# Performance work log

Hardware: AMD Instinct MI355X
Metric: run time of the kernel (lower is better)

Reference implementation:

```python
import jax, jax.numpy as jnp
import numpy as np

N_NODES = 4096
HIDDEN = 64
N_REL = 8
N_LAYERS = 2


def setup_inputs() -> dict:
    key = jax.random.key(0)
    k0, k1, k2, k3, k4 = jax.random.split(key, 5)
    node_embed = jax.random.normal(k0, (N_NODES + 1, HIDDEN), dtype=jnp.float32)
    w_self = jax.random.normal(k1, (N_LAYERS, HIDDEN, HIDDEN), dtype=jnp.float32) * 0.02
    w_rel = jax.random.normal(k2, (N_LAYERS, N_REL, HIDDEN, HIDDEN), dtype=jnp.float32) * 0.02
    # dense per-relation adjacency buffer [R, N, N]
    rel_adj = jax.random.uniform(k3, (N_REL, N_NODES, N_NODES), dtype=jnp.float32)
    keyword_ids = jax.random.randint(k4, (64, 32), 0, N_NODES + 1)  # pad id == N_NODES
    return {"node_embed": node_embed, "w_self": w_self, "w_rel": w_rel,
            "rel_adj": rel_adj, "keyword_ids": keyword_ids}


def reference(node_embed, w_self, w_rel, rel_adj, keyword_ids):
    num_nodes = rel_adj.shape[1]
    h = node_embed[:num_nodes]  # [N, D]
    for l in range(w_self.shape[0]):
        out = h @ w_self[l]                                   # self loop [N, D]
        msg = jnp.einsum('rnm,md->rnd', rel_adj, h)           # per-relation aggregation
        out = out + jnp.einsum('rnd,rde->ne', msg, w_rel[l])  # per-relation projection, summed over r
        h = jax.nn.relu(out)
    pad = jnp.zeros((1, h.shape[1]), dtype=h.dtype)
    full_plus_pad = jnp.concatenate([h, pad], axis=0)  # [N+1, D]
    return full_plus_pad[keyword_ids]                  # [B, K, D]
```

## Files before the change

kernel.cpp:

```cpp
#include <hip/hip_runtime.h>

#define N_NODES 4096
#define HID 64
#define NH (N_NODES * HID)

typedef float f32x4 __attribute__((ext_vector_type(4)));
typedef short s16x4 __attribute__((ext_vector_type(4)));
typedef short s16x8 __attribute__((ext_vector_type(8)));

__device__ __forceinline__ short f2bf(float f) {
    union { float f; unsigned u; } v; v.f = f;
    unsigned r = v.u + 0x7fffu + ((v.u >> 16) & 1u);
    return (short)(r >> 16);
}

__global__ __launch_bounds__(256) void proj_kernel(
    const float* __restrict__ h, const float* __restrict__ w_self_l,
    const float* __restrict__ w_rel_l, float* __restrict__ S,
    short* __restrict__ BT)
{
    __shared__ float hs[64][65];
    __shared__ float wt[64][64];
    const int tid = threadIdx.x;
    const int mb = blockIdx.x;
    const int p = blockIdx.y;
    const float* w = (p < 8) ? (w_rel_l + p * 64 * 64) : w_self_l;

    #pragma unroll
    for (int i = 0; i < 4; ++i) {
        int idx4 = tid + 256 * i;
        int row = idx4 >> 4, c = idx4 & 15;
        float4 v = *((const float4*)(h + (size_t)(mb * 64 + row) * HID) + c);
        hs[row][c * 4 + 0] = v.x; hs[row][c * 4 + 1] = v.y;
        hs[row][c * 4 + 2] = v.z; hs[row][c * 4 + 3] = v.w;
    }
    #pragma unroll
    for (int i = 0; i < 4; ++i) {
        int idx4 = tid + 256 * i;
        ((float4*)wt)[idx4] = ((const float4*)w)[idx4];
    }
    __syncthreads();

    const int m = tid & 63;
    const int eb = (tid >> 6) * 16;
    float acc[16];
    #pragma unroll
    for (int j = 0; j < 16; ++j) acc[j] = 0.f;

    #pragma unroll 4
    for (int d = 0; d < 64; ++d) {
        float hv = hs[m][d];
        const float4* wr = (const float4*)&wt[d][eb];
        float4 w0 = wr[0], w1 = wr[1], w2 = wr[2], w3 = wr[3];
        acc[0]  += hv * w0.x; acc[1]  += hv * w0.y; acc[2]  += hv * w0.z; acc[3]  += hv * w0.w;
        acc[4]  += hv * w1.x; acc[5]  += hv * w1.y; acc[6]  += hv * w1.z; acc[7]  += hv * w1.w;
        acc[8]  += hv * w2.x; acc[9]  += hv * w2.y; acc[10] += hv * w2.z; acc[11] += hv * w2.w;
        acc[12] += hv * w3.x; acc[13] += hv * w3.y; acc[14] += hv * w3.z; acc[15] += hv * w3.w;
    }

    if (p < 8) {
        #pragma unroll
        for (int j = 0; j < 16; ++j)
            BT[(size_t)(p * 64 + eb + j) * N_NODES + mb * 64 + m] = f2bf(acc[j]);
    } else {
        #pragma unroll
        for (int j = 0; j < 16; ++j)
            S[(size_t)(mb * 64 + m) * HID + eb + j] = acc[j];
    }
}

__global__ __launch_bounds__(256, 4) void gemm_kernel(
    const float* __restrict__ A, const short* __restrict__ BT,
    float* __restrict__ msg)
{
    __shared__ __attribute__((aligned(16))) short As[2][64 * 72];
    __shared__ __attribute__((aligned(16))) short Bs[2][64 * 72];

    const int tid = threadIdx.x;
    const int gid = blockIdx.x;
    const int r  = gid & 7;
    const int rb = (gid >> 3) & 63;
    const int ks = gid >> 9;
    const int wave = tid >> 6, lane = tid & 63;
    const int quad = lane >> 4, l16 = lane & 15;

    const int rA = tid >> 4, cA = tid & 15;
    const int rB = tid >> 3, cB = tid & 7;
    const float* Ag = A  + ((size_t)r * N_NODES + rb * 64) * N_NODES + ks * 2048;
    const short* Bg = BT + ((size_t)r * 64) * N_NODES + ks * 2048;

    f32x4 acc[4];
    #pragma unroll
    for (int nb = 0; nb < 4; ++nb) acc[nb] = (f32x4){0.f, 0.f, 0.f, 0.f};

    f32x4 a_nx[4];
    s16x8 b_nx[2];
    auto load_tile = [&](int t) {
        const int k0 = t * 64;
        #pragma unroll
        for (int j = 0; j < 4; ++j)
            a_nx[j] = __builtin_nontemporal_load(
                (const f32x4*)(Ag + (size_t)(rA + 16 * j) * N_NODES + k0 + cA * 4));
        #pragma unroll
        for (int j = 0; j < 2; ++j)
            b_nx[j] = *(const s16x8*)(Bg + (size_t)(rB + 32 * j) * N_NODES + k0 + cB * 8);
    };
    auto write_tile = [&](int b) {
        #pragma unroll
        for (int j = 0; j < 4; ++j) {
            s16x4 av;
            av[0] = f2bf(a_nx[j][0]); av[1] = f2bf(a_nx[j][1]);
            av[2] = f2bf(a_nx[j][2]); av[3] = f2bf(a_nx[j][3]);
            *(s16x4*)&As[b][(rA + 16 * j) * 72 + cA * 4] = av;
        }
        #pragma unroll
        for (int j = 0; j < 2; ++j)
            *(s16x8*)&Bs[b][(rB + 32 * j) * 72 + cB * 8] = b_nx[j];
    };

    load_tile(0);
    write_tile(0);
    load_tile(1);
    asm volatile("s_waitcnt lgkmcnt(0)" ::: "memory");
    __builtin_amdgcn_s_barrier();

    #pragma unroll 2
    for (int t = 0; t < 32; ++t) {
        const int b = t & 1;
        #pragma unroll
        for (int s = 0; s < 2; ++s) {
            s16x8 af = *(const s16x8*)&As[b][(wave * 16 + l16) * 72 + s * 32 + quad * 8];
            #pragma unroll
            for (int nb = 0; nb < 4; ++nb) {
                s16x8 bfr = *(const s16x8*)&Bs[b][(nb * 16 + l16) * 72 + s * 32 + quad * 8];
                acc[nb] = __builtin_amdgcn_mfma_f32_16x16x32_bf16(af, bfr, acc[nb], 0, 0, 0);
            }
        }
        if (t < 31) {
            __builtin_amdgcn_sched_barrier(0);
            write_tile(b ^ 1);
            if (t < 30) load_tile(t + 2);
            asm volatile("s_waitcnt lgkmcnt(0)" ::: "memory");
            __builtin_amdgcn_s_barrier();
        }
    }

    float* mo = msg + ((size_t)(r * 2 + ks)) * NH;
    #pragma unroll
    for (int nb = 0; nb < 4; ++nb) {
        #pragma unroll
        for (int i = 0; i < 4; ++i) {
            int orow = rb * 64 + wave * 16 + quad * 4 + i;
            mo[(size_t)orow * HID + nb * 16 + l16] = acc[nb][i];
        }
    }
}

__global__ __launch_bounds__(256) void relu_kernel(
    const float* __restrict__ S, const float* __restrict__ msg, float* __restrict__ hout)
{
    int i = blockIdx.x * 256 + threadIdx.x;
    float4 s = ((const float4*)S)[i];
    #pragma unroll
    for (int p = 0; p < 16; ++p) {
        float4 m = ((const float4*)(msg + (size_t)p * NH))[i];
        s.x += m.x; s.y += m.y; s.z += m.z; s.w += m.w;
    }
    float4 o;
    o.x = fmaxf(s.x, 0.f); o.y = fmaxf(s.y, 0.f);
    o.z = fmaxf(s.z, 0.f); o.w = fmaxf(s.w, 0.f);
    ((float4*)hout)[i] = o;
}

__global__ __launch_bounds__(256) void gather_kernel(
    const float* __restrict__ h2, const int* __restrict__ kw, float* __restrict__ out)
{
    int e = blockIdx.x * 256 + threadIdx.x;
    int ki = e >> 6, d = e & 63;
    int id = kw[ki];
    out[e] = ((unsigned)id < (unsigned)N_NODES) ? h2[(size_t)id * HID + d] : 0.f;
}

extern "C" void kernel_launch(void* const* d_in, const int* in_sizes, int n_in,
                              void* d_out, int out_size, void* d_ws, size_t ws_size,
                              hipStream_t stream) {
    const float* node_embed = (const float*)d_in[0];
    const float* w_self     = (const float*)d_in[1];
    const float* w_rel      = (const float*)d_in[2];
    const float* rel_adj    = (const float*)d_in[3];
    const int*   kw         = (const int*)d_in[4];
    float* out = (float*)d_out;

    float* msg = (float*)d_ws;
    float* S   = msg + 16 * NH;
    float* h1  = S + NH;
    float* h2  = h1 + NH;
    short* BT  = (short*)(h2 + NH);

    const float* hin = node_embed;
    float* houts[2] = {h1, h2};
    for (int l = 0; l < 2; ++l) {
        proj_kernel<<<dim3(64, 9), 256, 0, stream>>>(
            hin, w_self + (size_t)l * 64 * 64, w_rel + (size_t)l * 8 * 64 * 64, S, BT);
        gemm_kernel<<<1024, 256, 0, stream>>>(rel_adj, BT, msg);
        relu_kernel<<<256, 256, 0, stream>>>(S, msg, houts[l]);
        hin = houts[l];
    }
    gather_kernel<<<512, 256, 0, stream>>>(h2, kw, out);
}
```

Before: 821.0 us.

## Drop split-K in adjacency GEMM, stream 16-row phases through full K

```diff
diff --git a/kernel.cpp b/kernel.cpp
--- a/kernel.cpp
+++ b/kernel.cpp
@@ -3,6 +3,7 @@
 #define N_NODES 4096
 #define HID 64
 #define NH (N_NODES * HID)
+#define NPART 8
 
 typedef float f32x4 __attribute__((ext_vector_type(4)));
 typedef short s16x4 __attribute__((ext_vector_type(4)));
@@ -69,53 +70,51 @@
     }
 }
 
-__global__ __launch_bounds__(256, 4) void gemm_kernel(
+__global__ __launch_bounds__(256, 3) void gemm_kernel(
     const float* __restrict__ A, const short* __restrict__ BT,
     float* __restrict__ msg)
 {
-    __shared__ __attribute__((aligned(16))) short As[2][64 * 72];
-    __shared__ __attribute__((aligned(16))) short Bs[2][64 * 72];
+    __shared__ __attribute__((aligned(16))) short As[2][16 * 136];
+    __shared__ __attribute__((aligned(16))) short Bs[2][64 * 136];
 
     const int tid = threadIdx.x;
     const int gid = blockIdx.x;
     const int r  = gid & 7;
-    const int rb = (gid >> 3) & 63;
-    const int ks = gid >> 9;
+    const int rb = gid >> 3;
     const int wave = tid >> 6, lane = tid & 63;
     const int quad = lane >> 4, l16 = lane & 15;
 
     const int rA = tid >> 4, cA = tid & 15;
-    const int rB = tid >> 3, cB = tid & 7;
-    const float* Ag = A  + ((size_t)r * N_NODES + rb * 64) * N_NODES + ks * 2048;
-    const short* Bg = BT + ((size_t)r * 64) * N_NODES + ks * 2048;
-
-    f32x4 acc[4];
-    #pragma unroll
-    for (int nb = 0; nb < 4; ++nb) acc[nb] = (f32x4){0.f, 0.f, 0.f, 0.f};
-
-    f32x4 a_nx[4];
-    s16x8 b_nx[2];
-    auto load_tile = [&](int t) {
-        const int k0 = t * 64;
-        #pragma unroll
-        for (int j = 0; j < 4; ++j)
-            a_nx[j] = __builtin_nontemporal_load(
-                (const f32x4*)(Ag + (size_t)(rA + 16 * j) * N_NODES + k0 + cA * 4));
-        #pragma unroll
-        for (int j = 0; j < 2; ++j)
-            b_nx[j] = *(const s16x8*)(Bg + (size_t)(rB + 32 * j) * N_NODES + k0 + cB * 8);
+    const int rB = tid >> 2, cB = tid & 3;
+    const float* Ag = A  + ((size_t)r * N_NODES + rb * 64) * N_NODES;
+    const short* Bg = BT + (size_t)r * 64 * N_NODES;
+
+    f32x4 acc = (f32x4){0.f, 0.f, 0.f, 0.f};
+
+    f32x4 a_nx[2];
+    s16x8 b_nx[4];
+    auto load_tile = [&](int u) {
+        const int ph = u >> 5;
+        const int k0 = (u & 31) * 128;
+        #pragma unroll
+        for (int s = 0; s < 2; ++s)
+            a_nx[s] = __builtin_nontemporal_load(
+                (const f32x4*)(Ag + (size_t)(ph * 16 + rA) * N_NODES + k0 + cA * 4 + s * 64));
+        #pragma unroll
+        for (int s = 0; s < 4; ++s)
+            b_nx[s] = *(const s16x8*)(Bg + (size_t)rB * N_NODES + k0 + cB * 8 + s * 32);
     };
     auto write_tile = [&](int b) {
         #pragma unroll
-        for (int j = 0; j < 4; ++j) {
+        for (int s = 0; s < 2; ++s) {
             s16x4 av;
-            av[0] = f2bf(a_nx[j][0]); av[1] = f2bf(a_nx[j][1]);
-            av[2] = f2bf(a_nx[j][2]); av[3] = f2bf(a_nx[j][3]);
-            *(s16x4*)&As[b][(rA + 16 * j) * 72 + cA * 4] = av;
-        }
-        #pragma unroll
-        for (int j = 0; j < 2; ++j)
-            *(s16x8*)&Bs[b][(rB + 32 * j) * 72 + cB * 8] = b_nx[j];
+            av[0] = f2bf(a_nx[s][0]); av[1] = f2bf(a_nx[s][1]);
+            av[2] = f2bf(a_nx[s][2]); av[3] = f2bf(a_nx[s][3]);
+            *(s16x4*)&As[b][rA * 136 + cA * 4 + s * 64] = av;
+        }
+        #pragma unroll
+        for (int s = 0; s < 4; ++s)
+            *(s16x8*)&Bs[b][rB * 136 + cB * 8 + s * 32] = b_nx[s];
     };
 
     load_tile(0);
@@ -124,36 +123,34 @@
     asm volatile("s_waitcnt lgkmcnt(0)" ::: "memory");
     __builtin_amdgcn_s_barrier();
 
+    float* mo = msg + (size_t)r * NH;
+
     #pragma unroll 2
-    for (int t = 0; t < 32; ++t) {
-        const int b = t & 1;
-        #pragma unroll
-        for (int s = 0; s < 2; ++s) {
-            s16x8 af = *(const s16x8*)&As[b][(wave * 16 + l16) * 72 + s * 32 + quad * 8];
+    for (int u = 0; u < 128; ++u) {
+        const int b = u & 1;
+        #pragma unroll
+        for (int kk = 0; kk < 4; ++kk) {
+            s16x8 af  = *(const s16x8*)&As[b][l16 * 136 + kk * 32 + quad * 8];
+            s16x8 bfr = *(const s16x8*)&Bs[b][(wave * 16 + l16) * 136 + kk * 32 + quad * 8];
+            acc = __builtin_amdgcn_mfma_f32_16x16x32_bf16(af, bfr, acc, 0, 0, 0);
+        }
+        if ((u & 31) == 31) {
+            const int ph = u >> 5;
             #pragma unroll
-            for (int nb = 0; nb < 4; ++nb) {
-                s16x8 bfr = *(const s16x8*)&Bs[b][(nb * 16 + l16) * 72 + s * 32 + quad * 8];
-                acc[nb] = __builtin_amdgcn_mfma_f32_16x16x32_bf16(af, bfr, acc[nb], 0, 0, 0);
+            for (int i = 0; i < 4; ++i) {
+                int orow = rb * 64 + ph * 16 + quad * 4 + i;
+                mo[(size_t)orow * HID + wave * 16 + l16] = acc[i];
             }
-        }
-        if (t < 31) {
+            acc = (f32x4){0.f, 0.f, 0.f, 0.f};
+        }
+        if (u < 127) {
             __builtin_amdgcn_sched_barrier(0);
             write_tile(b ^ 1);
-            if (t < 30) load_tile(t + 2);
+            if (u < 126) load_tile(u + 2);
             asm volatile("s_waitcnt lgkmcnt(0)" ::: "memory");
             __builtin_amdgcn_s_barrier();
         }
     }
-
-    float* mo = msg + ((size_t)(r * 2 + ks)) * NH;
-    #pragma unroll
-    for (int nb = 0; nb < 4; ++nb) {
-        #pragma unroll
-        for (int i = 0; i < 4; ++i) {
-            int orow = rb * 64 + wave * 16 + quad * 4 + i;
-            mo[(size_t)orow * HID + nb * 16 + l16] = acc[nb][i];
-        }
-    }
 }
 
 __global__ __launch_bounds__(256) void relu_kernel(
@@ -162,7 +159,7 @@
     int i = blockIdx.x * 256 + threadIdx.x;
     float4 s = ((const float4*)S)[i];
     #pragma unroll
-    for (int p = 0; p < 16; ++p) {
+    for (int p = 0; p < NPART; ++p) {
         float4 m = ((const float4*)(msg + (size_t)p * NH))[i];
         s.x += m.x; s.y += m.y; s.z += m.z; s.w += m.w;
     }
@@ -192,7 +189,7 @@
     float* out = (float*)d_out;
 
     float* msg = (float*)d_ws;
-    float* S   = msg + 16 * NH;
+    float* S   = msg + NPART * NH;
     float* h1  = S + NH;
     float* h2  = h1 + NH;
     short* BT  = (short*)(h2 + NH);
@@ -202,7 +199,7 @@
     for (int l = 0; l < 2; ++l) {
         proj_kernel<<<dim3(64, 9), 256, 0, stream>>>(
             hin, w_self + (size_t)l * 64 * 64, w_rel + (size_t)l * 8 * 64 * 64, S, BT);
-        gemm_kernel<<<1024, 256, 0, stream>>>(rel_adj, BT, msg);
+        gemm_kernel<<<512, 256, 0, stream>>>(rel_adj, BT, msg);
         relu_kernel<<<256, 256, 0, stream>>>(S, msg, houts[l]);
         hin = houts[l];
     }
```

Result: no change. 828.7 us (+0.9%).
